# Kernel tuning notes

Hardware: AMD Instinct MI355X
Metric: run time of the kernel (lower is better)

The kernel has to match this reference:

```python
import jax, jax.numpy as jnp
import numpy as np

ALPHA = 0.2  # leakyrelu negative slope
NEG_INF = -1.0e12


def setup_inputs() -> dict:
    key = jax.random.key(0)
    k1, k2, k3, k4, k5 = jax.random.split(key, 5)
    B, N, C_in, C_out = 8, 2048, 256, 256
    inp = jax.random.normal(k1, (B, N, C_in), dtype=jnp.float32)
    adj = jax.random.randint(k2, (N, N), 0, 2, dtype=jnp.int32)
    # xavier_uniform with gain=1.414 for (C_in, C_out)
    limit = 1.414 * np.sqrt(6.0 / (C_in + C_out))
    W1 = jax.random.uniform(k3, (C_in, C_out), jnp.float32, -limit, limit)
    W2 = jax.random.uniform(k4, (C_in, C_out), jnp.float32, -limit, limit)
    W3 = jax.random.uniform(k5, (C_in, C_out), jnp.float32, -limit, limit)
    return {"inp": inp, "adj": adj, "W1": W1, "W2": W2, "W3": W3}


def reference(inp, adj, W1, W2, W3):
    # inp: [B,N,Cin], adj: [N,N], W*: [Cin,Cout]
    h1 = jnp.einsum('bnc,cd->bnd', inp, W1)  # [B,N,Cout] queries
    h2 = jnp.einsum('bnc,cd->bnd', inp, W2)  # [B,N,Cout] keys
    h3 = jnp.einsum('bnc,cd->bnd', inp, W3)  # [B,N,Cout] values
    e = jnp.einsum('bnd,bmd->bnm', h1, h2)   # [B,N,N] scores
    e = jax.nn.leaky_relu(e, ALPHA)
    e = jnp.where(adj[None, :, :] > 0, e, NEG_INF)
    attention = jax.nn.softmax(e, axis=-1)   # dropout p=0 / eval mode -> identity
    h_prime = jnp.einsum('bnm,bmd->bnd', attention, h3)
    return jax.nn.relu(h_prime)  # concat=True
```

## Files before the change

### kernel.cpp

```cpp
#include <hip/hip_runtime.h>

typedef __bf16 bf16_t;
typedef __bf16 bf16x4 __attribute__((ext_vector_type(4)));
typedef __bf16 bf16x8 __attribute__((ext_vector_type(8)));
typedef float floatx4 __attribute__((ext_vector_type(4)));

#define S_H   (8 * 2048 * 256)

__device__ inline void split_hl(float v, bf16_t& hi, bf16_t& lo) {
    hi = (bf16_t)v;
    lo = (bf16_t)(v - (float)hi);
}

__global__ void adjbits_kernel(const int* __restrict__ adj, unsigned* __restrict__ bits) {
    int id = blockIdx.x * 256 + threadIdx.x;
    const int* p = adj + (size_t)id * 32;
    unsigned w = 0;
#pragma unroll
    for (int j = 0; j < 32; j += 4) {
        int4 v = *(const int4*)(p + j);
        w |= (v.x > 0 ? 1u : 0u) << j;
        w |= (v.y > 0 ? 1u : 0u) << (j + 1);
        w |= (v.z > 0 ? 1u : 0u) << (j + 2);
        w |= (v.w > 0 ? 1u : 0u) << (j + 3);
    }
    bits[id] = w;
}

__global__ void wtrans_kernel(const float* __restrict__ W1,
                              const float* __restrict__ W2,
                              const float* __restrict__ W3,
                              bf16_t* __restrict__ Wthi, bf16_t* __restrict__ Wtlo) {
    __shared__ float T[64 * 68];
    const int zi = blockIdx.z;
    const float* W = (zi == 0) ? W1 : ((zi == 1) ? W2 : W3);
    bf16_t* ohi = Wthi + zi * 256 * 256;
    bf16_t* olo = Wtlo + zi * 256 * 256;
    const int c0 = blockIdx.x * 64, d0 = blockIdx.y * 64;
    const int tid = threadIdx.x;
#pragma unroll
    for (int i = 0; i < 4; i++) {
        int idx = i * 256 + tid;
        int r = idx >> 4, c4 = (idx & 15) * 4;
        floatx4 v = *(const floatx4*)(W + (c0 + r) * 256 + d0 + c4);
        *(floatx4*)(&T[r * 68 + c4]) = v;
    }
    __syncthreads();
#pragma unroll
    for (int i = 0; i < 4; i++) {
        int idx = i * 256 + tid;
        int rd = idx & 63, cc4 = (idx >> 6) * 4;
        bf16x4 vh, vl;
#pragma unroll
        for (int ii = 0; ii < 4; ii++) {
            float v = T[(cc4 + ii) * 68 + rd];
            bf16_t h, l; split_hl(v, h, l);
            vh[ii] = h; vl[ii] = l;
        }
        *(bf16x4*)(ohi + (d0 + rd) * 256 + c0 + cc4) = vh;
        *(bf16x4*)(olo + (d0 + rd) * 256 + c0 + cc4) = vl;
    }
}

__global__ __launch_bounds__(256) void proj_kernel(
    const float* __restrict__ X,
    const bf16_t* __restrict__ Wthi, const bf16_t* __restrict__ Wtlo,
    bf16_t* __restrict__ H1hi, bf16_t* __restrict__ H1lo,
    bf16_t* __restrict__ H2hi, bf16_t* __restrict__ H2lo,
    bf16_t* __restrict__ H3t) {
    __shared__ bf16_t Xh[64 * 40], Xl[64 * 40];
    __shared__ bf16_t Wh[256 * 40], Wl[256 * 40];
    const int z = blockIdx.y;
    const int row0 = blockIdx.x * 64;
    const int tid = threadIdx.x;
    const int w = tid >> 6, lane = tid & 63;
    const int m = lane & 15, q = lane >> 4;
    const bf16_t* Wzh = Wthi + z * 256 * 256;
    const bf16_t* Wzl = Wtlo + z * 256 * 256;

    floatx4 acc[16];
#pragma unroll
    for (int i = 0; i < 16; i++) acc[i] = (floatx4){0.f, 0.f, 0.f, 0.f};

    for (int c0 = 0; c0 < 256; c0 += 32) {
#pragma unroll
        for (int i = 0; i < 2; i++) {
            int idx = i * 256 + tid;
            int r = idx >> 3, c4 = (idx & 7) * 4;
            floatx4 v = *(const floatx4*)(X + (size_t)(row0 + r) * 256 + c0 + c4);
            bf16x4 vh, vl;
#pragma unroll
            for (int ii = 0; ii < 4; ii++) {
                bf16_t h, l; split_hl(v[ii], h, l);
                vh[ii] = h; vl[ii] = l;
            }
            *(bf16x4*)(&Xh[r * 40 + c4]) = vh;
            *(bf16x4*)(&Xl[r * 40 + c4]) = vl;
        }
#pragma unroll
        for (int i = 0; i < 4; i++) {
            int idx = i * 256 + tid;
            int d = idx >> 2, c8 = (idx & 3) * 8;
            *(bf16x8*)(&Wh[d * 40 + c8]) = *(const bf16x8*)(Wzh + d * 256 + c0 + c8);
            *(bf16x8*)(&Wl[d * 40 + c8]) = *(const bf16x8*)(Wzl + d * 256 + c0 + c8);
        }
        __syncthreads();
        bf16x8 ah = *(const bf16x8*)(&Xh[(w * 16 + m) * 40 + q * 8]);
        bf16x8 al = *(const bf16x8*)(&Xl[(w * 16 + m) * 40 + q * 8]);
#pragma unroll
        for (int nt = 0; nt < 16; nt++) {
            bf16x8 bh = *(const bf16x8*)(&Wh[(nt * 16 + m) * 40 + q * 8]);
            bf16x8 bl = *(const bf16x8*)(&Wl[(nt * 16 + m) * 40 + q * 8]);
            acc[nt] = __builtin_amdgcn_mfma_f32_16x16x32_bf16(ah, bh, acc[nt], 0, 0, 0);
            acc[nt] = __builtin_amdgcn_mfma_f32_16x16x32_bf16(ah, bl, acc[nt], 0, 0, 0);
            acc[nt] = __builtin_amdgcn_mfma_f32_16x16x32_bf16(al, bh, acc[nt], 0, 0, 0);
        }
        __syncthreads();
    }
    const int rbase = row0 + w * 16 + q * 4;
    if (z < 2) {
        bf16_t* Hhi = (z == 0) ? H1hi : H2hi;
        bf16_t* Hlo = (z == 0) ? H1lo : H2lo;
#pragma unroll
        for (int nt = 0; nt < 16; nt++)
#pragma unroll
            for (int r = 0; r < 4; r++) {
                bf16_t h, l; split_hl(acc[nt][r], h, l);
                int off = (rbase + r) * 256 + nt * 16 + m;
                Hhi[off] = h;
                Hlo[off] = l;
            }
    } else {
#pragma unroll
        for (int nt = 0; nt < 16; nt++)
#pragma unroll
            for (int r = 0; r < 4; r++) {
                int token = rbase + r;
                int b = token >> 11, n = token & 2047;
                H3t[(size_t)(b * 256 + nt * 16 + m) * 2048 + n] = (bf16_t)acc[nt][r];
            }
    }
}

__global__ __launch_bounds__(512, 2) void attn_kernel(
    const bf16_t* __restrict__ H1hi, const bf16_t* __restrict__ H1lo,
    const bf16_t* __restrict__ H2hi, const bf16_t* __restrict__ H2lo,
    const bf16_t* __restrict__ H3t, const unsigned* __restrict__ adjbits,
    float* __restrict__ Opart, float* __restrict__ mpart, float* __restrict__ lpart,
    int klen) {
    __shared__ bf16_t Kl[2][32 * 260];
    __shared__ bf16_t Vl[256 * 40];
    __shared__ bf16_t Pl[8][16 * 40];

    const int b = blockIdx.y;
    const int q0 = blockIdx.x * 128;
    const int kz = blockIdx.z;
    const int tid = threadIdx.x;
    const int w = tid >> 6, lane = tid & 63;
    const int m = lane & 15, q = lane >> 4;

    const bf16_t* qrh = H1hi + (size_t)(b * 2048 + q0 + w * 16 + m) * 256;
    const bf16_t* qrl = H1lo + (size_t)(b * 2048 + q0 + w * 16 + m) * 256;
    bf16x8 qhi[8], qlo[8];
#pragma unroll
    for (int ck = 0; ck < 8; ck++) {
        qhi[ck] = *(const bf16x8*)(qrh + ck * 32 + q * 8);
        qlo[ck] = *(const bf16x8*)(qrl + ck * 32 + q * 8);
    }

    float m_run[4], l_run[4];
#pragma unroll
    for (int r = 0; r < 4; r++) { m_run[r] = -3.0e38f; l_run[r] = 0.f; }
    floatx4 o[16];
#pragma unroll
    for (int i = 0; i < 16; i++) o[i] = (floatx4){0.f, 0.f, 0.f, 0.f};

    const unsigned* bitrow[4];
#pragma unroll
    for (int r = 0; r < 4; r++)
        bitrow[r] = adjbits + (size_t)(q0 + w * 16 + q * 4 + r) * 64;

    bf16x8 rkh[2], rkl[2], rvv[2];
    const int kbeg = kz * klen, kend = kbeg + klen;

#pragma unroll
    for (int i = 0; i < 2; i++) {
        int ci = i * 512 + tid;
        int kr = ci >> 5, c8 = (ci & 31) * 8;
        rkh[i] = *(const bf16x8*)(H2hi + (size_t)(b * 2048 + kbeg + kr) * 256 + c8);
        rkl[i] = *(const bf16x8*)(H2lo + (size_t)(b * 2048 + kbeg + kr) * 256 + c8);
        int d = ci >> 2, k8 = (ci & 3) * 8;
        rvv[i] = *(const bf16x8*)(H3t + (size_t)(b * 256 + d) * 2048 + kbeg + k8);
    }

    for (int k0 = kbeg; k0 < kend; k0 += 32) {
        __syncthreads();
#pragma unroll
        for (int i = 0; i < 2; i++) {
            int ci = i * 512 + tid;
            int kr = ci >> 5, c8 = (ci & 31) * 8;
            *(bf16x8*)(&Kl[0][kr * 260 + c8]) = rkh[i];
            *(bf16x8*)(&Kl[1][kr * 260 + c8]) = rkl[i];
            int d = ci >> 2, k8 = (ci & 3) * 8;
            *(bf16x8*)(&Vl[d * 40 + k8]) = rvv[i];
        }
        __syncthreads();
        if (k0 + 32 < kend) {
            int kn = k0 + 32;
#pragma unroll
            for (int i = 0; i < 2; i++) {
                int ci = i * 512 + tid;
                int kr = ci >> 5, c8 = (ci & 31) * 8;
                rkh[i] = *(const bf16x8*)(H2hi + (size_t)(b * 2048 + kn + kr) * 256 + c8);
                rkl[i] = *(const bf16x8*)(H2lo + (size_t)(b * 2048 + kn + kr) * 256 + c8);
                int d = ci >> 2, k8 = (ci & 3) * 8;
                rvv[i] = *(const bf16x8*)(H3t + (size_t)(b * 256 + d) * 2048 + kn + k8);
            }
        }

        floatx4 s[2];
#pragma unroll
        for (int t = 0; t < 2; t++) {
            floatx4 accs = (floatx4){0.f, 0.f, 0.f, 0.f};
#pragma unroll
            for (int ck = 0; ck < 8; ck++) {
                bf16x8 khi = *(const bf16x8*)(&Kl[0][(t * 16 + m) * 260 + ck * 32 + q * 8]);
                bf16x8 klo = *(const bf16x8*)(&Kl[1][(t * 16 + m) * 260 + ck * 32 + q * 8]);
                accs = __builtin_amdgcn_mfma_f32_16x16x32_bf16(qhi[ck], khi, accs, 0, 0, 0);
                accs = __builtin_amdgcn_mfma_f32_16x16x32_bf16(qhi[ck], klo, accs, 0, 0, 0);
                accs = __builtin_amdgcn_mfma_f32_16x16x32_bf16(qlo[ck], khi, accs, 0, 0, 0);
            }
            s[t] = accs;
        }

        unsigned aw[4];
#pragma unroll
        for (int r = 0; r < 4; r++) aw[r] = bitrow[r][k0 >> 5];
        float p[2][4], tmax[4];
#pragma unroll
        for (int r = 0; r < 4; r++) tmax[r] = -3.0e38f;
#pragma unroll
        for (int t = 0; t < 2; t++)
#pragma unroll
            for (int r = 0; r < 4; r++) {
                float v = s[t][r];
                v = (v > 0.f) ? v : 0.2f * v;
                v = ((aw[r] >> (t * 16 + m)) & 1u) ? v : -1.0e12f;
                p[t][r] = v;
                tmax[r] = fmaxf(tmax[r], v);
            }
#pragma unroll
        for (int off = 1; off < 16; off <<= 1)
#pragma unroll
            for (int r = 0; r < 4; r++)
                tmax[r] = fmaxf(tmax[r], __shfl_xor(tmax[r], off, 64));

        int rise = 0;
        float mnew[4];
#pragma unroll
        for (int r = 0; r < 4; r++) {
            mnew[r] = fmaxf(m_run[r], tmax[r]);
            rise |= (mnew[r] > m_run[r]);
        }
        if (__any(rise)) {
#pragma unroll
            for (int r = 0; r < 4; r++) {
                float alpha = __expf(m_run[r] - mnew[r]);
                m_run[r] = mnew[r];
                l_run[r] *= alpha;
#pragma unroll
                for (int nt = 0; nt < 16; nt++) o[nt][r] *= alpha;
            }
        }
        float rsum[4];
#pragma unroll
        for (int r = 0; r < 4; r++) {
            float e0 = __expf(p[0][r] - m_run[r]);
            float e1 = __expf(p[1][r] - m_run[r]);
            p[0][r] = e0; p[1][r] = e1;
            rsum[r] = e0 + e1;
        }
#pragma unroll
        for (int off = 1; off < 16; off <<= 1)
#pragma unroll
            for (int r = 0; r < 4; r++)
                rsum[r] += __shfl_xor(rsum[r], off, 64);
#pragma unroll
        for (int r = 0; r < 4; r++) l_run[r] += rsum[r];

#pragma unroll
        for (int t = 0; t < 2; t++)
#pragma unroll
            for (int r = 0; r < 4; r++)
                Pl[w][(q * 4 + r) * 40 + t * 16 + m] = (bf16_t)p[t][r];
        bf16x8 pf = *(const bf16x8*)(&Pl[w][m * 40 + q * 8]);

#pragma unroll
        for (int nt = 0; nt < 16; nt++) {
            bf16x8 vf = *(const bf16x8*)(&Vl[(nt * 16 + m) * 40 + q * 8]);
            o[nt] = __builtin_amdgcn_mfma_f32_16x16x32_bf16(pf, vf, o[nt], 0, 0, 0);
        }
    }

    const int rowg = kz * 16384 + b * 2048 + q0 + w * 16 + q * 4;
#pragma unroll
    for (int nt = 0; nt < 16; nt++)
#pragma unroll
        for (int r = 0; r < 4; r++)
            Opart[(size_t)(rowg + r) * 256 + nt * 16 + m] = o[nt][r];
    if (m == 0) {
#pragma unroll
        for (int r = 0; r < 4; r++) {
            mpart[rowg + r] = m_run[r];
            lpart[rowg + r] = l_run[r];
        }
    }
}

__global__ __launch_bounds__(256) void merge_kernel(
    const float* __restrict__ Opart, const float* __restrict__ mpart,
    const float* __restrict__ lpart, float* __restrict__ out, int S) {
    int gid = blockIdx.x * 256 + threadIdx.x;
    int row = gid >> 6, c4 = (gid & 63) * 4;
    float M = -3.0e38f;
    for (int s = 0; s < S; s++) M = fmaxf(M, mpart[s * 16384 + row]);
    float denom = 0.f;
    float4 acc = make_float4(0.f, 0.f, 0.f, 0.f);
    for (int s = 0; s < S; s++) {
        float sc = __expf(mpart[s * 16384 + row] - M);
        denom += lpart[s * 16384 + row] * sc;
        float4 v = *(const float4*)(Opart + ((size_t)(s * 16384 + row)) * 256 + c4);
        acc.x += v.x * sc; acc.y += v.y * sc; acc.z += v.z * sc; acc.w += v.w * sc;
    }
    float inv = 1.f / denom;
    float4 r;
    r.x = fmaxf(acc.x * inv, 0.f);
    r.y = fmaxf(acc.y * inv, 0.f);
    r.z = fmaxf(acc.z * inv, 0.f);
    r.w = fmaxf(acc.w * inv, 0.f);
    *(float4*)(out + (size_t)row * 256 + c4) = r;
}

extern "C" void kernel_launch(void* const* d_in, const int* in_sizes, int n_in,
                              void* d_out, int out_size, void* d_ws, size_t ws_size,
                              hipStream_t stream) {
    const float* X   = (const float*)d_in[0];
    const int*   adj = (const int*)d_in[1];
    const float* W1  = (const float*)d_in[2];
    const float* W2  = (const float*)d_in[3];
    const float* W3  = (const float*)d_in[4];
    float* out = (float*)d_out;

    char* ws = (char*)d_ws;
    bf16_t* H1hi = (bf16_t*)(ws + (size_t)0 * S_H * 2);
    bf16_t* H1lo = (bf16_t*)(ws + (size_t)1 * S_H * 2);
    bf16_t* H2hi = (bf16_t*)(ws + (size_t)2 * S_H * 2);
    bf16_t* H2lo = (bf16_t*)(ws + (size_t)3 * S_H * 2);
    bf16_t* H3t  = (bf16_t*)(ws + (size_t)4 * S_H * 2);
    size_t off = (size_t)5 * S_H * 2;
    bf16_t* Wthi = (bf16_t*)(ws + off);
    bf16_t* Wtlo = (bf16_t*)(ws + off + 393216);
    float* mpart = (float*)(ws + off);
    float* lpart = (float*)(ws + off + 131072);
    unsigned* adjb = (unsigned*)(ws + off + 786432);
    size_t opart_off = off + 786432 + 524288;
    const size_t need2 = opart_off + (size_t)2 * 16384 * 256 * 4;

    int S = (ws_size >= need2) ? 2 : 1;
    float* Opart = (S == 2) ? (float*)(ws + opart_off) : out;

    adjbits_kernel<<<512, 256, 0, stream>>>(adj, adjb);
    wtrans_kernel<<<dim3(4, 4, 3), 256, 0, stream>>>(W1, W2, W3, Wthi, Wtlo);
    proj_kernel<<<dim3(256, 3), 256, 0, stream>>>(X, Wthi, Wtlo,
                                                  H1hi, H1lo, H2hi, H2lo, H3t);
    attn_kernel<<<dim3(16, 8, S), 512, 0, stream>>>(H1hi, H1lo, H2hi, H2lo, H3t,
                                                    adjb, Opart, mpart, lpart, 2048 / S);
    merge_kernel<<<4096, 256, 0, stream>>>(Opart, mpart, lpart, out, S);
}
```

Baseline: 243.4 us.

## Compute softmax row sums via MFMA, raise occupancy, and split keys four ways

The per-row softmax denominator is now built with an MFMA of the bf16 probability fragment against a vector of ones, replacing the cross-lane shuffle reduction. This uses the bf16-rounded probabilities, which matches what is multiplied with V. Launch bounds ask for 4 blocks per CU instead of 2, which squeezes registers and may cause spills. When the workspace is large enough the key dimension is split into 4 partitions instead of 2, with lpart relocated to make room. This adds more grid parallelism at the cost of more partial-output traffic in the merge.

```diff
diff --git a/kernel.cpp b/kernel.cpp
--- a/kernel.cpp
+++ b/kernel.cpp
@@ -142,7 +142,7 @@
     }
 }
 
-__global__ __launch_bounds__(512, 2) void attn_kernel(
+__global__ __launch_bounds__(512, 4) void attn_kernel(
     const bf16_t* __restrict__ H1hi, const bf16_t* __restrict__ H1lo,
     const bf16_t* __restrict__ H2hi, const bf16_t* __restrict__ H2lo,
     const bf16_t* __restrict__ H3t, const unsigned* __restrict__ adjbits,
@@ -168,9 +168,14 @@
         qlo[ck] = *(const bf16x8*)(qrl + ck * 32 + q * 8);
     }
 
-    float m_run[4], l_run[4];
-#pragma unroll
-    for (int r = 0; r < 4; r++) { m_run[r] = -3.0e38f; l_run[r] = 0.f; }
+    bf16x8 vones;
+#pragma unroll
+    for (int i = 0; i < 8; i++) vones[i] = (bf16_t)1.0f;
+
+    float m_run[4];
+#pragma unroll
+    for (int r = 0; r < 4; r++) m_run[r] = -3.0e38f;
+    floatx4 l_acc = (floatx4){0.f, 0.f, 0.f, 0.f};
     floatx4 o[16];
 #pragma unroll
     for (int i = 0; i < 16; i++) o[i] = (floatx4){0.f, 0.f, 0.f, 0.f};
@@ -267,26 +272,16 @@
             for (int r = 0; r < 4; r++) {
                 float alpha = __expf(m_run[r] - mnew[r]);
                 m_run[r] = mnew[r];
-                l_run[r] *= alpha;
+                l_acc[r] *= alpha;
 #pragma unroll
                 for (int nt = 0; nt < 16; nt++) o[nt][r] *= alpha;
             }
         }
-        float rsum[4];
-#pragma unroll
-        for (int r = 0; r < 4; r++) {
-            float e0 = __expf(p[0][r] - m_run[r]);
-            float e1 = __expf(p[1][r] - m_run[r]);
-            p[0][r] = e0; p[1][r] = e1;
-            rsum[r] = e0 + e1;
-        }
-#pragma unroll
-        for (int off = 1; off < 16; off <<= 1)
+#pragma unroll
+        for (int t = 0; t < 2; t++)
 #pragma unroll
             for (int r = 0; r < 4; r++)
-                rsum[r] += __shfl_xor(rsum[r], off, 64);
-#pragma unroll
-        for (int r = 0; r < 4; r++) l_run[r] += rsum[r];
+                p[t][r] = __expf(p[t][r] - m_run[r]);
 
 #pragma unroll
         for (int t = 0; t < 2; t++)
@@ -295,6 +290,8 @@
                 Pl[w][(q * 4 + r) * 40 + t * 16 + m] = (bf16_t)p[t][r];
         bf16x8 pf = *(const bf16x8*)(&Pl[w][m * 40 + q * 8]);
 
+        l_acc = __builtin_amdgcn_mfma_f32_16x16x32_bf16(pf, vones, l_acc, 0, 0, 0);
+
 #pragma unroll
         for (int nt = 0; nt < 16; nt++) {
             bf16x8 vf = *(const bf16x8*)(&Vl[(nt * 16 + m) * 40 + q * 8]);
@@ -312,7 +309,7 @@
 #pragma unroll
         for (int r = 0; r < 4; r++) {
             mpart[rowg + r] = m_run[r];
-            lpart[rowg + r] = l_run[r];
+            lpart[rowg + r] = l_acc[r];
         }
     }
 }
@@ -361,13 +358,14 @@
     bf16_t* Wthi = (bf16_t*)(ws + off);
     bf16_t* Wtlo = (bf16_t*)(ws + off + 393216);
     float* mpart = (float*)(ws + off);
-    float* lpart = (float*)(ws + off + 131072);
+    float* lpart = (float*)(ws + off + 262144);
     unsigned* adjb = (unsigned*)(ws + off + 786432);
     size_t opart_off = off + 786432 + 524288;
     const size_t need2 = opart_off + (size_t)2 * 16384 * 256 * 4;
-
-    int S = (ws_size >= need2) ? 2 : 1;
-    float* Opart = (S == 2) ? (float*)(ws + opart_off) : out;
+    const size_t need4 = opart_off + (size_t)4 * 16384 * 256 * 4;
+
+    int S = (ws_size >= need4) ? 4 : ((ws_size >= need2) ? 2 : 1);
+    float* Opart = (S > 1) ? (float*)(ws + opart_off) : out;
 
     adjbits_kernel<<<512, 256, 0, stream>>>(adj, adjb);
     wtrans_kernel<<<dim3(4, 4, 3), 256, 0, stream>>>(W1, W2, W3, Wthi, Wtlo);
```

Measured after the change: 698.0 us. 2.87x slower.
